# Performance work log

Measured on AMD Instinct MI355X. Metric: run time of the kernel, lower is better.

The kernel has to match this reference:

```python
import jax, jax.numpy as jnp
import numpy as np
from jax import lax

B, C, H, W = 16, 512, 64, 64
DIM_OUT = C
IN_CH = DIM_OUT * 2          # 1024
OUT_CH = DIM_OUT // 2 * 3    # 768
ATT_DIM = DIM_OUT // 2       # 256
DN = ('NCHW', 'OIHW', 'NCHW')


def setup_inputs() -> dict:
    key = jax.random.key(0)
    k = jax.random.split(key, 6)
    x = jax.random.normal(k[0], (B, C, H, W), dtype=jnp.float32)
    y = jax.random.normal(k[1], (B, C, H, W), dtype=jnp.float32)
    # DSConv = depthwise 3x3 (groups=IN_CH) + pointwise 1x1, both with bias.
    dw_w = jax.random.normal(k[2], (IN_CH, 1, 3, 3), dtype=jnp.float32) * 0.05
    dw_b = jax.random.normal(k[3], (IN_CH,), dtype=jnp.float32) * 0.02
    pw_w = jax.random.normal(k[4], (OUT_CH, IN_CH, 1, 1), dtype=jnp.float32) * 0.02
    pw_b = jax.random.normal(k[5], (OUT_CH,), dtype=jnp.float32) * 0.02
    return {"x": x, "y": y, "dw_w": dw_w, "dw_b": dw_b, "pw_w": pw_w, "pw_b": pw_b}


def reference(x, y, dw_w, dw_b, pw_w, pw_b):
    b, c, h, w = x.shape
    inp = jnp.concatenate([x, y], axis=1)  # [b, 2c, h, w]
    # depthwise 3x3, padding=1
    t = lax.conv_general_dilated(inp, dw_w, (1, 1), 'SAME',
                                 dimension_numbers=DN,
                                 feature_group_count=IN_CH)
    t = t + dw_b[None, :, None, None]
    # pointwise 1x1
    fm = lax.conv_general_dilated(t, pw_w, (1, 1), 'SAME', dimension_numbers=DN)
    fm = fm + pw_b[None, :, None, None]                      # [b, 3*att, h, w]
    # rearrange 'b (qkv c) h w -> qkv b h c w'
    qkv = fm.reshape(b, 3, ATT_DIM, h, w).transpose(1, 0, 3, 2, 4)  # [3,b,h,c,w]
    Q, K, V = qkv[0], qkv[1], qkv[2]                         # each [b,h,c,w]
    dots = jnp.einsum('bhcw,bhdw->bhcd', Q, K)               # unscaled, [b,h,c,c]
    attn = jax.nn.softmax(dots, axis=-1)
    out = jnp.einsum('bhcd,bhdw->bhcw', attn, V)             # [b,h,c,w]
    # torch .view(b, -1, h, w): plain row-major reshape of [b,h,c,w]
    return out.reshape(b, -1, h, w)                          # [b, c, h, w]
```

## Files before the change

kernel.cpp:

```cpp
#include <hip/hip_runtime.h>

typedef unsigned short u16;
typedef float f32x4 __attribute__((ext_vector_type(4)));
typedef short s16x8 __attribute__((ext_vector_type(8)));
typedef _Float16 f16x8 __attribute__((ext_vector_type(8)));

static __device__ __forceinline__ u16 f2h(float f) {
  return __builtin_bit_cast(u16, (_Float16)f);
}

static __device__ __forceinline__ f32x4 MFMA(s16x8 a, s16x8 b, f32x4 c) {
  return __builtin_amdgcn_mfma_f32_16x16x32_f16(
      __builtin_bit_cast(f16x8, a), __builtin_bit_cast(f16x8, b), c, 0, 0, 0);
}

__global__ __launch_bounds__(256) void convw_kernel(
    const float* __restrict__ w, u16* __restrict__ wb) {
  const int i = (blockIdx.x * 256 + threadIdx.x) * 4;
  const f32x4 v = *(const f32x4*)(w + i);
  ushort4 o;
  o.x = f2h(v.x); o.y = f2h(v.y); o.z = f2h(v.z); o.w = f2h(v.w);
  *(ushort4*)(wb + i) = o;
}

__global__ __launch_bounds__(256, 4) void dwconv_kernel(
    const float* __restrict__ x, const float* __restrict__ y,
    const float* __restrict__ dww, const float* __restrict__ dwb,
    u16* __restrict__ Tt) {
  __shared__ __align__(16) u16 tile[4][64][68];
  __shared__ float wl[640];
  const int icb = blockIdx.x, hb = blockIdx.y, b = blockIdx.z;
  const int t = threadIdx.x;

  for (int i = t; i < 576; i += 256) wl[i] = dww[icb * 576 + i];
  if (t < 64) wl[576 + t] = dwb[icb * 64 + t];
  __syncthreads();

  const int wq = t & 15;
  const int cs = t >> 4;
  const int h0 = hb * 4;

#pragma unroll
  for (int cc = 0; cc < 4; ++cc) {
    const int ch = cs * 4 + cc;
    const int ic = icb * 64 + ch;
    const float* src = (ic < 512) ? (x + (size_t)(b * 512 + ic) * 4096)
                                  : (y + (size_t)(b * 512 + (ic - 512)) * 4096);
    f32x4 r[6];
    float lm[6], lp[6];
#pragma unroll
    for (int j = 0; j < 6; ++j) {
      const int hh = h0 - 1 + j;
      f32x4 v = {0.f, 0.f, 0.f, 0.f};
      if (hh >= 0 && hh <= 63) v = *(const f32x4*)(src + hh * 64 + wq * 4);
      r[j] = v;
      const float l = __shfl_up(v.w, 1, 16);
      const float rr = __shfl_down(v.x, 1, 16);
      lm[j] = (wq == 0) ? 0.f : l;
      lp[j] = (wq == 15) ? 0.f : rr;
    }
    const float w00 = wl[ch * 9 + 0], w01 = wl[ch * 9 + 1], w02 = wl[ch * 9 + 2];
    const float w10 = wl[ch * 9 + 3], w11 = wl[ch * 9 + 4], w12 = wl[ch * 9 + 5];
    const float w20 = wl[ch * 9 + 6], w21 = wl[ch * 9 + 7], w22 = wl[ch * 9 + 8];
    const float bias = wl[576 + ch];
#pragma unroll
    for (int ro = 0; ro < 4; ++ro) {
      f32x4 acc = {bias, bias, bias, bias};
#pragma unroll
      for (int d = 0; d < 3; ++d) {
        const int j = ro + d;
        const float wa = (d == 0) ? w00 : (d == 1) ? w10 : w20;
        const float wb_ = (d == 0) ? w01 : (d == 1) ? w11 : w21;
        const float wc = (d == 0) ? w02 : (d == 1) ? w12 : w22;
        acc.x += wa * lm[j]   + wb_ * r[j].x + wc * r[j].y;
        acc.y += wa * r[j].x  + wb_ * r[j].y + wc * r[j].z;
        acc.z += wa * r[j].y  + wb_ * r[j].z + wc * r[j].w;
        acc.w += wa * r[j].z  + wb_ * r[j].w + wc * lp[j];
      }
      ushort4 o;
      o.x = f2h(acc.x); o.y = f2h(acc.y); o.z = f2h(acc.z); o.w = f2h(acc.w);
      *(ushort4*)&tile[ro][ch][wq * 4] = o;
    }
  }
  __syncthreads();

  const int icq = t & 15;
  const size_t outb = (size_t)b * 4096 * 1024 + (size_t)icb * 64 + icq * 4;
#pragma unroll
  for (int it = 0; it < 16; ++it) {
    const int ro = it >> 2;
    const int w = (it & 3) * 16 + (t >> 4);
    ushort4 o;
    o.x = tile[ro][icq * 4 + 0][w];
    o.y = tile[ro][icq * 4 + 1][w];
    o.z = tile[ro][icq * 4 + 2][w];
    o.w = tile[ro][icq * 4 + 3][w];
    const size_t p = (size_t)(h0 + ro) * 64 + w;
    *(ushort4*)(Tt + outb + p * 1024) = o;
  }
}

__global__ __launch_bounds__(256) void pwgemm_kernel(
    const u16* __restrict__ W, const float* __restrict__ pwb,
    const u16* __restrict__ Tt, u16* __restrict__ FM) {
  __shared__ __align__(16) u16 sA[128 * 64];
  __shared__ __align__(16) u16 sB[128 * 64];
  const int b = blockIdx.z;
  const int m0 = blockIdx.y * 128, n0 = blockIdx.x * 128;
  const int t = threadIdx.x, wv = t >> 6, lane = t & 63;
  const int mw = (wv >> 1) * 64, nw = (wv & 1) * 64;
  const int l15 = lane & 15, lq = lane >> 4;
  const int rsw = (l15 & 7) << 3;
  f32x4 acc[4][4] = {};
  const u16* Wb = W + (size_t)m0 * 1024;
  const u16* Tb = Tt + ((size_t)b * 4096 + n0) * 1024;
  for (int k0 = 0; k0 < 1024; k0 += 64) {
    s16x8 av[4], bv[4];
#pragma unroll
    for (int jj = 0; jj < 4; ++jj) {
      const int c = jj * 256 + t;
      const int row = c >> 3, col = (c & 7) * 8;
      av[jj] = *(const s16x8*)(Wb + (size_t)row * 1024 + k0 + col);
      bv[jj] = *(const s16x8*)(Tb + (size_t)row * 1024 + k0 + col);
    }
    __syncthreads();
#pragma unroll
    for (int jj = 0; jj < 4; ++jj) {
      const int c = jj * 256 + t;
      const int row = c >> 3, col = (c & 7) * 8;
      const int sc = col ^ ((row & 7) << 3);
      *(s16x8*)&sA[row * 64 + sc] = av[jj];
      *(s16x8*)&sB[row * 64 + sc] = bv[jj];
    }
    __syncthreads();
#pragma unroll
    for (int ks = 0; ks < 2; ++ks) {
      s16x8 af[4], bfv[4];
      const int cbase = (ks * 32 + lq * 8) ^ rsw;
#pragma unroll
      for (int i = 0; i < 4; ++i)
        af[i] = *(const s16x8*)&sA[(mw + i * 16 + l15) * 64 + cbase];
#pragma unroll
      for (int j = 0; j < 4; ++j)
        bfv[j] = *(const s16x8*)&sB[(nw + j * 16 + l15) * 64 + cbase];
#pragma unroll
      for (int i = 0; i < 4; ++i)
#pragma unroll
        for (int j = 0; j < 4; ++j)
          acc[i][j] = MFMA(af[i], bfv[j], acc[i][j]);
    }
  }
#pragma unroll
  for (int i = 0; i < 4; ++i)
#pragma unroll
    for (int r = 0; r < 4; ++r) {
      const int oc = m0 + mw + i * 16 + lq * 4 + r;
      const float bias = pwb[oc];
#pragma unroll
      for (int j = 0; j < 4; ++j) {
        const int p = n0 + nw + j * 16 + l15;
        FM[((size_t)b * 768 + oc) * 4096 + p] = f2h(acc[i][j][r] + bias);
      }
    }
}

__global__ __launch_bounds__(256) void attn_kernel(
    const u16* __restrict__ FM, float* __restrict__ out) {
  __shared__ __align__(16) u16 sKV[16384];
  __shared__ __align__(16) u16 sP[16384];
  const int sb = blockIdx.x, h = blockIdx.y, b = blockIdx.z;
  const int t = threadIdx.x, wv = t >> 6, lane = t & 63;
  const int l15 = lane & 15, lq = lane >> 4;
  const int rsw = (l15 & 7) << 3;
  const u16* fmb = FM + (size_t)b * 768 * 4096;
  const int hofs = h * 64;

#pragma unroll
  for (int it = 0; it < 8; ++it) {
    const int c = it * 256 + t;
    const int d = c >> 3, w0 = (c & 7) * 8;
    const s16x8 kv = *(const s16x8*)(fmb + (size_t)(256 + d) * 4096 + hofs + w0);
    *(s16x8*)&sKV[d * 64 + (w0 ^ ((d & 7) << 3))] = kv;
  }
  const int qrow = sb * 64 + wv * 16 + l15;
  s16x8 qf[2];
#pragma unroll
  for (int ks = 0; ks < 2; ++ks)
    qf[ks] = *(const s16x8*)(fmb + (size_t)qrow * 4096 + hofs + ks * 32 + lq * 8);
  __syncthreads();

  f32x4 sreg[16] = {};
#pragma unroll
  for (int ks = 0; ks < 2; ++ks) {
    const int cbase = (ks * 32 + lq * 8) ^ rsw;
#pragma unroll
    for (int j = 0; j < 16; ++j) {
      const s16x8 kf = *(const s16x8*)&sKV[(j * 16 + l15) * 64 + cbase];
      sreg[j] = MFMA(qf[ks], kf, sreg[j]);
    }
  }

  float inv[4], mx[4];
#pragma unroll
  for (int r = 0; r < 4; ++r) {
    float v = -3.4e38f;
#pragma unroll
    for (int j = 0; j < 16; ++j) v = fmaxf(v, sreg[j][r]);
#pragma unroll
    for (int mk = 1; mk < 16; mk <<= 1) v = fmaxf(v, __shfl_xor(v, mk, 64));
    mx[r] = v;
  }
#pragma unroll
  for (int r = 0; r < 4; ++r) {
    float ss = 0.f;
#pragma unroll
    for (int j = 0; j < 16; ++j) {
      const float e = __expf(fminf(sreg[j][r] - mx[r], 0.f));
      sreg[j][r] = e;
      ss += e;
    }
#pragma unroll
    for (int mk = 1; mk < 16; mk <<= 1) ss += __shfl_xor(ss, mk, 64);
    inv[r] = 1.0f / fmaxf(ss, 1e-30f);
  }
#pragma unroll
  for (int r = 0; r < 4; ++r) {
    const int row = wv * 16 + lq * 4 + r;
    const int s = (row & 7) << 3;
#pragma unroll
    for (int j = 0; j < 16; ++j)
      sP[row * 256 + ((j * 16 + l15) ^ s)] = f2h(sreg[j][r] * inv[r]);
  }
  __syncthreads();

#pragma unroll
  for (int it = 0; it < 8; ++it) {
    const int c = it * 256 + t;
    const int d = c >> 3, w0 = (c & 7) * 8;
    const s16x8 vv = *(const s16x8*)(fmb + (size_t)(512 + d) * 4096 + hofs + w0);
#pragma unroll
    for (int j = 0; j < 8; ++j) {
      const int rr = w0 + j;
      sKV[rr * 256 + (d ^ ((rr & 7) << 3))] = (u16)vv[j];
    }
  }
  __syncthreads();

  f32x4 o[4] = {};
#pragma unroll
  for (int kk = 0; kk < 8; ++kk) {
    const int cbase = (kk * 32 + lq * 8) ^ rsw;
    const s16x8 pf = *(const s16x8*)&sP[(wv * 16 + l15) * 256 + cbase];
#pragma unroll
    for (int j = 0; j < 4; ++j) {
      const s16x8 vf = *(const s16x8*)&sKV[(j * 16 + l15) * 256 + cbase];
      o[j] = MFMA(pf, vf, o[j]);
    }
  }
  const size_t ob = (((size_t)b * 64 + h) * 256 + sb * 64 + wv * 16) * 64;
#pragma unroll
  for (int j = 0; j < 4; ++j)
#pragma unroll
    for (int r = 0; r < 4; ++r)
      out[ob + (size_t)(lq * 4 + r) * 64 + j * 16 + l15] = o[j][r];
}

extern "C" void kernel_launch(void* const* d_in, const int* in_sizes, int n_in,
                              void* d_out, int out_size, void* d_ws, size_t ws_size,
                              hipStream_t stream) {
  (void)in_sizes; (void)n_in; (void)out_size; (void)ws_size;
  const float* x   = (const float*)d_in[0];
  const float* y   = (const float*)d_in[1];
  const float* dww = (const float*)d_in[2];
  const float* dwb = (const float*)d_in[3];
  const float* pww = (const float*)d_in[4];
  const float* pwb = (const float*)d_in[5];
  u16* Tt   = (u16*)d_ws;
  u16* FM   = Tt + (size_t)16 * 4096 * 1024;
  u16* Wb16 = FM + (size_t)16 * 768 * 4096;
  float* out = (float*)d_out;

  convw_kernel<<<dim3(768), 256, 0, stream>>>(pww, Wb16);
  dwconv_kernel<<<dim3(16, 16, 16), 256, 0, stream>>>(x, y, dww, dwb, Tt);
  pwgemm_kernel<<<dim3(32, 6, 16), 256, 0, stream>>>(Wb16, pwb, Tt, FM);
  attn_kernel<<<dim3(4, 64, 16), 256, 0, stream>>>(FM, out);
}
```

Baseline: 556.4 us.

## Use direct global-to-LDS loads for GEMM and attention K tiles, reswizzle V

Replaces the register-staged global loads followed by shared-memory stores in the pointwise GEMM and the attention K load with the global_load_lds builtin, which writes straight into LDS with an XOR swizzle built into the per-lane source addresses. This removes the VGPR round trip and the separate LDS write instructions and simplifies the loop to a sync, load, sync pattern. It also changes the V tile swizzle to mix in higher row bits to cut bank conflicts on the transposed V reads. Nothing overlaps the loads with compute, since there is no double buffering, and correctness depends on the builtin's LDS addressing matching the expected layout.

```diff
diff --git a/kernel.cpp b/kernel.cpp
--- a/kernel.cpp
+++ b/kernel.cpp
@@ -12,6 +12,12 @@
 static __device__ __forceinline__ f32x4 MFMA(s16x8 a, s16x8 b, f32x4 c) {
   return __builtin_amdgcn_mfma_f32_16x16x32_f16(
       __builtin_bit_cast(f16x8, a), __builtin_bit_cast(f16x8, b), c, 0, 0, 0);
+}
+
+static __device__ __forceinline__ void g2l16(const u16* g, u16* l) {
+  __builtin_amdgcn_global_load_lds(
+      (const __attribute__((address_space(1))) void*)g,
+      (__attribute__((address_space(3))) void*)l, 16, 0, 0);
 }
 
 __global__ __launch_bounds__(256) void convw_kernel(
@@ -112,25 +118,18 @@
   const int l15 = lane & 15, lq = lane >> 4;
   const int rsw = (l15 & 7) << 3;
   f32x4 acc[4][4] = {};
-  const u16* Wb = W + (size_t)m0 * 1024;
-  const u16* Tb = Tt + ((size_t)b * 4096 + n0) * 1024;
+  const int r8 = lane >> 3;
+  const int colsw = 8 * ((lane & 7) ^ r8);
+  const u16* gA = W + ((size_t)m0 + wv * 8 + r8) * 1024 + colsw;
+  const u16* gB = Tt + ((size_t)b * 4096 + n0 + wv * 8 + r8) * 1024 + colsw;
+  u16* lA = sA + wv * 512;
+  u16* lB = sB + wv * 512;
   for (int k0 = 0; k0 < 1024; k0 += 64) {
-    s16x8 av[4], bv[4];
+    __syncthreads();
 #pragma unroll
     for (int jj = 0; jj < 4; ++jj) {
-      const int c = jj * 256 + t;
-      const int row = c >> 3, col = (c & 7) * 8;
-      av[jj] = *(const s16x8*)(Wb + (size_t)row * 1024 + k0 + col);
-      bv[jj] = *(const s16x8*)(Tb + (size_t)row * 1024 + k0 + col);
-    }
-    __syncthreads();
-#pragma unroll
-    for (int jj = 0; jj < 4; ++jj) {
-      const int c = jj * 256 + t;
-      const int row = c >> 3, col = (c & 7) * 8;
-      const int sc = col ^ ((row & 7) << 3);
-      *(s16x8*)&sA[row * 64 + sc] = av[jj];
-      *(s16x8*)&sB[row * 64 + sc] = bv[jj];
+      g2l16(gA + (size_t)jj * 32 * 1024 + k0, lA + jj * 2048);
+      g2l16(gB + (size_t)jj * 32 * 1024 + k0, lB + jj * 2048);
     }
     __syncthreads();
 #pragma unroll
@@ -175,13 +174,14 @@
   const u16* fmb = FM + (size_t)b * 768 * 4096;
   const int hofs = h * 64;
 
-#pragma unroll
-  for (int it = 0; it < 8; ++it) {
-    const int c = it * 256 + t;
-    const int d = c >> 3, w0 = (c & 7) * 8;
-    const s16x8 kv = *(const s16x8*)(fmb + (size_t)(256 + d) * 4096 + hofs + w0);
-    *(s16x8*)&sKV[d * 64 + (w0 ^ ((d & 7) << 3))] = kv;
-  }
+  const int r8 = lane >> 3;
+  const int colsw = 8 * ((lane & 7) ^ r8);
+  const u16* gK = fmb + ((size_t)(256 + wv * 8 + r8)) * 4096 + hofs + colsw;
+  u16* lK = sKV + wv * 512;
+#pragma unroll
+  for (int it = 0; it < 8; ++it)
+    g2l16(gK + (size_t)it * 32 * 4096, lK + it * 2048);
+
   const int qrow = sb * 64 + wv * 16 + l15;
   s16x8 qf[2];
 #pragma unroll
@@ -241,7 +241,8 @@
 #pragma unroll
     for (int j = 0; j < 8; ++j) {
       const int rr = w0 + j;
-      sKV[rr * 256 + (d ^ ((rr & 7) << 3))] = (u16)vv[j];
+      const int s = ((rr & 7) ^ ((rr >> 3) & 7)) << 3;
+      sKV[rr * 256 + (d ^ s)] = (u16)vv[j];
     }
   }
   __syncthreads();
@@ -249,11 +250,13 @@
   f32x4 o[4] = {};
 #pragma unroll
   for (int kk = 0; kk < 8; ++kk) {
-    const int cbase = (kk * 32 + lq * 8) ^ rsw;
-    const s16x8 pf = *(const s16x8*)&sP[(wv * 16 + l15) * 256 + cbase];
+    const int cbase = kk * 32 + lq * 8;
+    const s16x8 pf = *(const s16x8*)&sP[(wv * 16 + l15) * 256 + (cbase ^ rsw)];
 #pragma unroll
     for (int j = 0; j < 4; ++j) {
-      const s16x8 vf = *(const s16x8*)&sKV[(j * 16 + l15) * 256 + cbase];
+      const int rr = j * 16 + l15;
+      const int vsw = ((rr & 7) ^ ((rr >> 3) & 7)) << 3;
+      const s16x8 vf = *(const s16x8*)&sKV[rr * 256 + (cbase ^ vsw)];
       o[j] = MFMA(pf, vf, o[j]);
     }
   }
```

New measurement: 532.9 us. 1.04x faster.
